# Kernel tuning notes

Measured on AMD Instinct MI355X. Metric: run time of the kernel, lower is better.

The kernel has to match this reference:

```python
import jax, jax.numpy as jnp
import numpy as np

H = 200
DT = 0.01
K = 100.0
C = 1.0
B = 131072


def setup_inputs() -> dict:
    key = jax.random.key(0)
    u_seq = jax.random.normal(key, (B, H), dtype=jnp.float32)
    x1_0 = jnp.zeros((B,), dtype=jnp.float32)
    v1_0 = jnp.ones((B,), dtype=jnp.float32)
    x2_0 = jnp.ones((B,), dtype=jnp.float32) * 2.0
    v2_0 = jnp.zeros((B,), dtype=jnp.float32)
    goal = jnp.ones((1,), dtype=jnp.float32) * 5.0
    return {"u_seq": u_seq, "x1_0": x1_0, "v1_0": v1_0,
            "x2_0": x2_0, "v2_0": v2_0, "goal": goal}


def _step(carry, u_t):
    x1, v1, x2, v2 = carry
    penetration = x1 + 1.0 - x2            # spring engages when box1 touches box2
    contact = jnp.maximum(penetration, 0.0)  # clamp(min=0)
    F_contact = -K * contact
    F1 = u_t + F_contact - C * v1
    F2 = -F_contact - C * v2
    v1 = v1 + F1 * DT
    v2 = v2 + F2 * DT
    x1 = x1 + v1 * DT
    x2 = x2 + v2 * DT
    return (x1, v1, x2, v2), None


def reference(u_seq, x1_0, v1_0, x2_0, v2_0, goal):
    # u_seq: [B, H]; states: [B]; goal: [1]
    (x1, v1, x2, v2), _ = jax.lax.scan(_step, (x1_0, v1_0, x2_0, v2_0),
                                       u_seq.T)  # scan over H steps
    loss = (x2 - goal) ** 2                # [B]
    return loss, x1, x2
```

## Files before the change

### kernel.cpp

```cpp
#include <hip/hip_runtime.h>

#define H_STEPS 200
#define DT 0.01f
#define K_SPRING 100.0f
#define NQ (H_STEPS / 4)

__device__ __forceinline__ void step(float u, float& x1, float& v1,
                                     float& x2, float& v2) {
    float pen     = x1 + 1.0f - x2;
    float contact = fmaxf(pen, 0.0f);
    float Fc      = -K_SPRING * contact;
    float F1      = u + Fc - v1;
    float F2      = -Fc - v2;
    v1 += F1 * DT;
    v2 += F2 * DT;
    x1 += v1 * DT;
    x2 += v2 * DT;
}

__global__ __launch_bounds__(256, 2)
void pushing_env_kernel(const float* __restrict__ u_seq,
                        const float* __restrict__ x1_0,
                        const float* __restrict__ v1_0,
                        const float* __restrict__ x2_0,
                        const float* __restrict__ v2_0,
                        const float* __restrict__ goal,
                        float* __restrict__ out, int B) {
    int b = blockIdx.x * blockDim.x + threadIdx.x;

    float x1 = x1_0[b];
    float v1 = v1_0[b];
    float x2 = x2_0[b];
    float v2 = v2_0[b];
    const float g = goal[0];

    const float4* u = reinterpret_cast<const float4*>(u_seq + (size_t)b * H_STEPS);

    float4 r[NQ];
    #pragma unroll
    for (int q = 0; q < NQ; ++q)
        r[q] = u[q];

    #pragma unroll
    for (int q = 0; q < NQ; ++q) {
        step(r[q].x, x1, v1, x2, v2);
        step(r[q].y, x1, v1, x2, v2);
        step(r[q].z, x1, v1, x2, v2);
        step(r[q].w, x1, v1, x2, v2);
    }

    float d = x2 - g;
    out[b]         = d * d;
    out[B + b]     = x1;
    out[2 * B + b] = x2;
}

extern "C" void kernel_launch(void* const* d_in, const int* in_sizes, int n_in,
                              void* d_out, int out_size, void* d_ws, size_t ws_size,
                              hipStream_t stream) {
    const float* u_seq = (const float*)d_in[0];
    const float* x1_0  = (const float*)d_in[1];
    const float* v1_0  = (const float*)d_in[2];
    const float* x2_0  = (const float*)d_in[3];
    const float* v2_0  = (const float*)d_in[4];
    const float* goal  = (const float*)d_in[5];
    float* out = (float*)d_out;

    const int B = in_sizes[1];
    const int block = 256;
    const int grid = B / block;
    pushing_env_kernel<<<grid, block, 0, stream>>>(u_seq, x1_0, v1_0, x2_0,
                                                   v2_0, goal, out, B);
}
```

Baseline: 23.79 us.

## Coalesce control-input loads and transpose through swizzled LDS per wave

Instead of each thread loading its own strided row of u_seq, lanes in a wave cooperatively load contiguous row segments (8 lanes per row) and transpose them through a per-wave XOR-swizzled LDS buffer in chunks. The last 8 steps are still read directly per thread. This aims to make the global loads coalesced and raise effective bandwidth. It adds LDS traffic, wave barriers and 32KB of shared memory per block, which may reduce occupancy.

```diff
diff --git a/kernel.cpp b/kernel.cpp
--- a/kernel.cpp
+++ b/kernel.cpp
@@ -3,7 +3,7 @@
 #define H_STEPS 200
 #define DT 0.01f
 #define K_SPRING 100.0f
-#define NQ (H_STEPS / 4)
+#define NCH 6
 
 __device__ __forceinline__ void step(float u, float& x1, float& v1,
                                      float& x2, float& v2) {
@@ -26,7 +26,12 @@
                         const float* __restrict__ v2_0,
                         const float* __restrict__ goal,
                         float* __restrict__ out, int B) {
-    int b = blockIdx.x * blockDim.x + threadIdx.x;
+    __shared__ float4 lds[4][64 * 8];
+    const int tid  = threadIdx.x;
+    const int wave = tid >> 6;
+    const int lane = tid & 63;
+    const int b0w  = blockIdx.x * 256 + wave * 64;
+    const int b    = b0w + lane;
 
     float x1 = x1_0[b];
     float v1 = v1_0[b];
@@ -34,20 +39,54 @@
     float v2 = v2_0[b];
     const float g = goal[0];
 
-    const float4* u = reinterpret_cast<const float4*>(u_seq + (size_t)b * H_STEPS);
+    const int lrow = lane >> 3;
+    const int lq   = lane & 7;
+    const float* ubase = u_seq + (size_t)b0w * H_STEPS;
 
-    float4 r[NQ];
+    float4 r[NCH][8];
     #pragma unroll
-    for (int q = 0; q < NQ; ++q)
-        r[q] = u[q];
+    for (int c = 0; c < NCH; ++c) {
+        #pragma unroll
+        for (int k = 0; k < 8; ++k) {
+            const int row = k * 8 + lrow;
+            r[c][k] = *reinterpret_cast<const float4*>(
+                ubase + (size_t)row * H_STEPS + (8 * c + lq) * 4);
+        }
+    }
+    const float4* urow = reinterpret_cast<const float4*>(
+        u_seq + (size_t)b * H_STEPS);
+    float4 t0 = urow[48];
+    float4 t1 = urow[49];
+
+    float4* lw = lds[wave];
 
     #pragma unroll
-    for (int q = 0; q < NQ; ++q) {
-        step(r[q].x, x1, v1, x2, v2);
-        step(r[q].y, x1, v1, x2, v2);
-        step(r[q].z, x1, v1, x2, v2);
-        step(r[q].w, x1, v1, x2, v2);
+    for (int c = 0; c < NCH; ++c) {
+        #pragma unroll
+        for (int k = 0; k < 8; ++k) {
+            const int R = k * 8 + lrow;
+            lw[R * 8 + (lq ^ lrow)] = r[c][k];
+        }
+        __builtin_amdgcn_wave_barrier();
+        #pragma unroll
+        for (int q = 0; q < 8; ++q) {
+            float4 u4 = lw[lane * 8 + (q ^ (lane & 7))];
+            step(u4.x, x1, v1, x2, v2);
+            step(u4.y, x1, v1, x2, v2);
+            step(u4.z, x1, v1, x2, v2);
+            step(u4.w, x1, v1, x2, v2);
+        }
+        __builtin_amdgcn_wave_barrier();
     }
+
+    step(t0.x, x1, v1, x2, v2);
+    step(t0.y, x1, v1, x2, v2);
+    step(t0.z, x1, v1, x2, v2);
+    step(t0.w, x1, v1, x2, v2);
+    step(t1.x, x1, v1, x2, v2);
+    step(t1.y, x1, v1, x2, v2);
+    step(t1.z, x1, v1, x2, v2);
+    step(t1.w, x1, v1, x2, v2);
 
     float d = x2 - g;
     out[b]         = d * d;
@@ -67,8 +106,7 @@
     float* out = (float*)d_out;
 
     const int B = in_sizes[1];
-    const int block = 256;
-    const int grid = B / block;
-    pushing_env_kernel<<<grid, block, 0, stream>>>(u_seq, x1_0, v1_0, x2_0,
-                                                   v2_0, goal, out, B);
+    const int grid = B / 256;
+    pushing_env_kernel<<<grid, 256, 0, stream>>>(u_seq, x1_0, v1_0, x2_0,
+                                                 v2_0, goal, out, B);
 }
```

Result: slower. 57.64 us (+142.3%).

## Split each row's input load across two lanes and exchange via shuffles

Applied to the files above, without the earlier changes.

Each batch row is now handled by a pair of lanes. Each lane loads half of the 200-step control sequence into registers, and the halves are exchanged with xor-1 shuffles, so both lanes run the full recurrence redundantly. This halves the per-thread register array, allows higher occupancy (launch bounds raised to 4), and makes adjacent lanes load contiguous memory. In exchange it doubles the thread count, duplicates the serial compute, and adds shuffle instructions on the dependent chain.

```diff
diff --git a/kernel.cpp b/kernel.cpp
--- a/kernel.cpp
+++ b/kernel.cpp
@@ -3,7 +3,7 @@
 #define H_STEPS 200
 #define DT 0.01f
 #define K_SPRING 100.0f
-#define NQ (H_STEPS / 4)
+#define NQH 25
 
 __device__ __forceinline__ void step(float u, float& x1, float& v1,
                                      float& x2, float& v2) {
@@ -18,7 +18,16 @@
     x2 += v2 * DT;
 }
 
-__global__ __launch_bounds__(256, 2)
+__device__ __forceinline__ float4 shfl_partner(float4 v) {
+    float4 r;
+    r.x = __shfl_xor(v.x, 1);
+    r.y = __shfl_xor(v.y, 1);
+    r.z = __shfl_xor(v.z, 1);
+    r.w = __shfl_xor(v.w, 1);
+    return r;
+}
+
+__global__ __launch_bounds__(256, 4)
 void pushing_env_kernel(const float* __restrict__ u_seq,
                         const float* __restrict__ x1_0,
                         const float* __restrict__ v1_0,
@@ -26,7 +35,9 @@
                         const float* __restrict__ v2_0,
                         const float* __restrict__ goal,
                         float* __restrict__ out, int B) {
-    int b = blockIdx.x * blockDim.x + threadIdx.x;
+    const int tid  = threadIdx.x;
+    const int half = tid & 1;
+    const int b    = blockIdx.x * 128 + (tid >> 1);
 
     float x1 = x1_0[b];
     float v1 = v1_0[b];
@@ -36,23 +47,36 @@
 
     const float4* u = reinterpret_cast<const float4*>(u_seq + (size_t)b * H_STEPS);
 
-    float4 r[NQ];
+    float4 r[NQH];
     #pragma unroll
-    for (int q = 0; q < NQ; ++q)
-        r[q] = u[q];
+    for (int q = 0; q < NQH; ++q)
+        r[q] = u[half * NQH + q];
 
     #pragma unroll
-    for (int q = 0; q < NQ; ++q) {
-        step(r[q].x, x1, v1, x2, v2);
-        step(r[q].y, x1, v1, x2, v2);
-        step(r[q].z, x1, v1, x2, v2);
-        step(r[q].w, x1, v1, x2, v2);
+    for (int q = 0; q < NQH; ++q) {
+        float4 p = shfl_partner(r[q]);
+        float4 u4 = half ? p : r[q];
+        step(u4.x, x1, v1, x2, v2);
+        step(u4.y, x1, v1, x2, v2);
+        step(u4.z, x1, v1, x2, v2);
+        step(u4.w, x1, v1, x2, v2);
+    }
+    #pragma unroll
+    for (int q = 0; q < NQH; ++q) {
+        float4 p = shfl_partner(r[q]);
+        float4 u4 = half ? r[q] : p;
+        step(u4.x, x1, v1, x2, v2);
+        step(u4.y, x1, v1, x2, v2);
+        step(u4.z, x1, v1, x2, v2);
+        step(u4.w, x1, v1, x2, v2);
     }
 
-    float d = x2 - g;
-    out[b]         = d * d;
-    out[B + b]     = x1;
-    out[2 * B + b] = x2;
+    if (half == 0) {
+        float d = x2 - g;
+        out[b]         = d * d;
+        out[B + b]     = x1;
+        out[2 * B + b] = x2;
+    }
 }
 
 extern "C" void kernel_launch(void* const* d_in, const int* in_sizes, int n_in,
@@ -65,10 +89,10 @@
     const float* v2_0  = (const float*)d_in[4];
     const float* goal  = (const float*)d_in[5];
     float* out = (float*)d_out;
+    (void)d_ws; (void)ws_size;
 
     const int B = in_sizes[1];
-    const int block = 256;
-    const int grid = B / block;
-    pushing_env_kernel<<<grid, block, 0, stream>>>(u_seq, x1_0, v1_0, x2_0,
-                                                   v2_0, goal, out, B);
+    const int grid = B / 128;
+    pushing_env_kernel<<<grid, 256, 0, stream>>>(u_seq, x1_0, v1_0, x2_0,
+                                                 v2_0, goal, out, B);
 }
```

Result: slower. 61.86 us (+160.1%).
